# Performance work log

Hardware: AMD Instinct MI355X
Metric: run time of the kernel (lower is better)

The kernel has to match this reference:

```python
import jax, jax.numpy as jnp
import numpy as np

B, T = 4096, 16384
KLEN = 50          # min(50, n_steps) with dt=1
REFRACTORY = 3.0   # self.refractory / self.dt


def setup_inputs() -> dict:
    key = jax.random.key(0)
    k1, = jax.random.split(key, 1)
    # scale so that v_reset + I_filtered/100 can cross v_th (=-55 vs reset -70)
    I_input = jax.random.normal(k1, (B, T), dtype=jnp.float32) * 2000.0
    return {
        "I_input": I_input,
        "tau_m": jnp.float32(10.0),
        "tau_s": jnp.float32(5.0),
        "v_th": jnp.float32(-55.0),
        "v_reset": jnp.float32(-70.0),
        "eta": jnp.float32(-5.0),
    }


def _srm_spikes(I_input, tau_m, tau_s, v_th, v_reset, eta):
    # synaptic kernel: (exp(-t/tau_m) - exp(-t/tau_s)) / sum
    t = jnp.arange(KLEN, dtype=jnp.float32)
    kernel = jnp.exp(-t / tau_m) - jnp.exp(-t / tau_s)
    kernel = kernel / (jnp.sum(kernel) + 1e-10)
    # 'same' convolution per trace (np.convolve semantics: kernel flipped)
    I_filt = jax.vmap(lambda x: jnp.convolve(x, kernel, mode="same"))(I_input)

    def step(ref, I_t):
        # ref: [B] refractory countdown; I_t: [B] filtered current at time t
        in_ref = ref > 0
        v_free = v_reset + I_t / 100.0
        spike = jnp.where(jnp.logical_and(~in_ref, v_free >= v_th), 1.0, 0.0)
        new_ref = jnp.where(in_ref, ref - 1.0,
                            jnp.where(spike > 0, REFRACTORY, 0.0))
        return new_ref, spike

    ref0 = jnp.zeros((I_input.shape[0],), dtype=jnp.float32)
    # original loop runs t = 1 .. n_steps-1; spikes[0] stays 0
    _, spikes_t = jax.lax.scan(step, ref0, jnp.swapaxes(I_filt[:, 1:], 0, 1))
    spikes = jnp.concatenate(
        [jnp.zeros((I_input.shape[0], 1), dtype=jnp.float32),
         jnp.swapaxes(spikes_t, 0, 1)], axis=1)
    return spikes


def reference(I_input, tau_m, tau_s, v_th, v_reset, eta):
    return _srm_spikes(I_input, tau_m, tau_s, v_th, v_reset, eta)
```

## Files before the change

kernel.cpp:

```cpp
#include <hip/hip_runtime.h>


#define TLEN  16384
#define NROWS 4096
#define GRP   256
#define NGRP  64
#define KLEN  50
#define WPB   4
#define TILEW 336
#define CHK   2
#define GPC   (NGRP / CHK)

#define WS_FLAGS_OFF 256
#define WS_NEED (WS_FLAGS_OFF + (size_t)NROWS * CHK * sizeof(int))

typedef float f4 __attribute__((ext_vector_type(4)));

__device__ __forceinline__ float uniformf(float x) {
    return __int_as_float(__builtin_amdgcn_readfirstlane(__float_as_int(x)));
}

__device__ __forceinline__ int map_compose(int first, int then) {
    int r = 0;
#pragma unroll
    for (int s = 0; s < 4; ++s) {
        int a = (first >> (2 * s)) & 3;
        int b = (then >> (2 * a)) & 3;
        r |= b << (2 * s);
    }
    return r;
}

__device__ float solve_thresh(float v_reset, float v_th) {
    auto tokey = [](float f) {
        unsigned u = __float_as_uint(f);
        return (u & 0x80000000u) ? ~u : (u | 0x80000000u);
    };
    auto fromkey = [](unsigned k) {
        unsigned u = (k & 0x80000000u) ? (k & 0x7FFFFFFFu) : ~k;
        return __uint_as_float(u);
    };
    const float maxf = 3.402823466e38f;
    unsigned lo = tokey(-maxf), hi = tokey(maxf);
    if (!((v_reset + maxf / 100.0f) >= v_th))
        return __uint_as_float(0x7F800000u);
    while (lo < hi) {
        unsigned mid = lo + ((hi - lo) >> 1);
        float a = fromkey(mid);
        if ((v_reset + a / 100.0f) >= v_th) hi = mid;
        else lo = mid + 1;
    }
    return fromkey(lo);
}

__global__ __launch_bounds__(64)
void setup_kernel(const float* __restrict__ p_tau_m,
                  const float* __restrict__ p_tau_s,
                  const float* __restrict__ p_v_th,
                  const float* __restrict__ p_v_reset,
                  float* __restrict__ wsf)
{
    const int lane = threadIdx.x & 63;
    const float tau_m   = p_tau_m[0];
    const float tau_s   = p_tau_s[0];

    float ft = (float)lane;
    float v = (lane < KLEN) ? (expf(-ft / tau_m) - expf(-ft / tau_s)) : 0.0f;

    float ksum = 0.0f;
    for (int t = 0; t < KLEN; ++t)
        ksum += __shfl(v, t, 64);
    const float kden = ksum + 1e-10f;
    const float kt = v / kden;

    if (lane < KLEN) wsf[lane] = kt;
    if (lane == 0)   wsf[KLEN] = solve_thresh(p_v_reset[0], p_v_th[0]);
}

__global__ __launch_bounds__(256)
void conv_kernel(const float* __restrict__ I,
                 const float* __restrict__ wsf,
                 float* __restrict__ out,
                 int* __restrict__ flags)
{
    __shared__ __align__(16) float tile[WPB][2][TILEW];

    const int lane  = threadIdx.x & 63;
    const int wid   = threadIdx.x >> 6;
    const int w     = blockIdx.x * WPB + wid;
    const int row   = w >> 1;
    const int chunk = w & 1;
    const int gi0   = chunk * GPC;

    float kt[KLEN];
#pragma unroll
    for (int t = 0; t < KLEN; ++t) kt[t] = wsf[t];
    const float athr = wsf[KLEN];

    const float* Irow = I + (size_t)row * TLEN;
    float* Orow = out + (size_t)row * TLEN;

    float Cv[4], Nv[4], Lv[4];
    {
        f4 a = *(const f4*)(Irow + (size_t)gi0 * GRP + 4 * lane);
        Cv[0] = a.x; Cv[1] = a.y; Cv[2] = a.z; Cv[3] = a.w;
        f4 c = *(const f4*)(Irow + (size_t)(gi0 + 1) * GRP + 4 * lane);
        Nv[0] = c.x; Nv[1] = c.y; Nv[2] = c.z; Nv[3] = c.w;
    }

    if (lane < 8) {
        f4 h;
        if (chunk == 0) h = (f4){0.0f, 0.0f, 0.0f, 0.0f};
        else            h = *(const f4*)(Irow + (size_t)gi0 * GRP - 32 + 4 * lane);
        *(f4*)&tile[wid][0][4 * lane] = h;
    }
    {
        f4 c; c.x = Cv[0]; c.y = Cv[1]; c.z = Cv[2]; c.w = Cv[3];
        *(f4*)&tile[wid][0][32 + 4 * lane] = c;
    }

    int rowflag = 0;

    for (int g = 0; g < GPC; ++g) {
        const int cur = g & 1;
        const int nxt = cur ^ 1;
        const int gi  = gi0 + g;

        if (gi + 2 < NGRP) {
            f4 a = *(const f4*)(Irow + (size_t)(gi + 2) * GRP + 4 * lane);
            Lv[0] = a.x; Lv[1] = a.y; Lv[2] = a.z; Lv[3] = a.w;
        } else {
            Lv[0] = Lv[1] = Lv[2] = Lv[3] = 0.0f;
        }

        f4 nv; nv.x = Nv[0]; nv.y = Nv[1]; nv.z = Nv[2]; nv.w = Nv[3];
        if (lane < 8)
            *(f4*)&tile[wid][cur][288 + 4 * lane] = nv;
        *(f4*)&tile[wid][nxt][32 + 4 * lane] = nv;
        if (lane >= 56) {
            f4 cv; cv.x = Cv[0]; cv.y = Cv[1]; cv.z = Cv[2]; cv.w = Cv[3];
            *(f4*)&tile[wid][nxt][4 * (lane - 56)] = cv;
        }

        f4 wv[15];
#pragma unroll
        for (int i = 0; i < 15; ++i)
            wv[i] = *(const f4*)&tile[wid][cur][4 * lane + 4 + 4 * i];
#define WIN(m) (wv[(m) >> 2][(m) & 3])

        float acc[4];
        acc[0] = acc[1] = acc[2] = acc[3] = 0.0f;
#pragma unroll
        for (int o = -25; o <= 27; ++o) {
            const float w2 = WIN(o + 28);
#pragma unroll
            for (int k = 0; k < 4; ++k) {
                const int jj = k + 24 - o;
                if (jj >= 0 && jj < KLEN)
                    acc[k] = fmaf(kt[jj], w2, acc[k]);
            }
        }
#undef WIN

        const int tb = gi * GRP + 4 * lane;
        int cand[4];
#pragma unroll
        for (int k = 0; k < 4; ++k)
            cand[k] = (acc[k] >= athr) ? 1 : 0;
        cand[0] &= (tb != 0);

        rowflag |= cand[0] | cand[1] | cand[2] | cand[3];

        f4 o0;
        o0.x = cand[0] ? 1.0f : 0.0f;
        o0.y = cand[1] ? 1.0f : 0.0f;
        o0.z = cand[2] ? 1.0f : 0.0f;
        o0.w = cand[3] ? 1.0f : 0.0f;
        __builtin_nontemporal_store(o0, (f4*)(Orow + tb));

#pragma unroll
        for (int j = 0; j < 4; ++j) { Cv[j] = Nv[j]; Nv[j] = Lv[j]; }
    }

    const unsigned long long anyb = __ballot(rowflag != 0);
    if (lane == 0) flags[w] = (anyb != 0ULL) ? 1 : 0;
}

__global__ __launch_bounds__(256)
void fixup_kernel(const int* __restrict__ flags,
                  float* __restrict__ out)
{
    const int lane = threadIdx.x & 63;
    const int wid  = threadIdx.x >> 6;
    const int row  = blockIdx.x * WPB + wid;

    if ((flags[2 * row] | flags[2 * row + 1]) == 0) return;

    float* Orow = out + (size_t)row * TLEN;
    int r0 = 0;

    for (int g = 0; g < NGRP; ++g) {
        f4 o = *(const f4*)(Orow + g * GRP + 4 * lane);
        int cand[4];
        cand[0] = (o.x != 0.0f);
        cand[1] = (o.y != 0.0f);
        cand[2] = (o.z != 0.0f);
        cand[3] = (o.w != 0.0f);

        const int cm = cand[0] | cand[1] | cand[2] | cand[3];
        const unsigned long long anyc = __ballot(cm != 0);
        if (anyc == 0ULL) { r0 = 0; continue; }

        int s0 = 0, s1 = 1, s2 = 2, s3 = 3;
#pragma unroll
        for (int k = 0; k < 4; ++k) {
            const int c3 = cand[k] ? 3 : 0;
            s0 = (s0 > 0) ? (s0 - 1) : c3;
            s1 = (s1 > 0) ? (s1 - 1) : c3;
            s2 = (s2 > 0) ? (s2 - 1) : c3;
            s3 = (s3 > 0) ? (s3 - 1) : c3;
        }
        int P = s0 | (s1 << 2) | (s2 << 4) | (s3 << 6);

#pragma unroll
        for (int d = 1; d < 64; d <<= 1) {
            const int prev = __shfl_up(P, d, 64);
            const int comp = map_compose(prev, P);
            P = (lane >= d) ? comp : P;
        }
        const int Pprev = __shfl_up(P, 1, 64);
        const int sin0  = (lane == 0) ? r0 : ((Pprev >> (2 * r0)) & 3);
        const int Pfull = __shfl(P, 63, 64);
        r0 = (Pfull >> (2 * r0)) & 3;

        int s = sin0;
        float sp[4];
#pragma unroll
        for (int k = 0; k < 4; ++k) {
            const int spike = (s == 0) & cand[k];
            sp[k] = spike ? 1.0f : 0.0f;
            s = (s > 0) ? (s - 1) : (cand[k] ? 3 : 0);
        }
        f4 o0; o0.x = sp[0]; o0.y = sp[1]; o0.z = sp[2]; o0.w = sp[3];
        *(f4*)(Orow + g * GRP + 4 * lane) = o0;
    }
}

__global__ __launch_bounds__(256)
void srm_kernel(const float* __restrict__ I,
                const float* __restrict__ p_tau_m,
                const float* __restrict__ p_tau_s,
                const float* __restrict__ p_v_th,
                const float* __restrict__ p_v_reset,
                float* __restrict__ out)
{
    __shared__ __align__(16) float tile[WPB][2][TILEW];

    const int lane = threadIdx.x & 63;
    const int wid  = threadIdx.x >> 6;
    const int row  = blockIdx.x * WPB + wid;

    const float tau_m   = p_tau_m[0];
    const float tau_s   = p_tau_s[0];
    const float v_th    = p_v_th[0];
    const float v_reset = p_v_reset[0];

    float ku[KLEN];
    float ksum = 0.0f;
#pragma unroll
    for (int t = 0; t < KLEN; ++t) {
        float ft = (float)t;
        float v = expf(-ft / tau_m) - expf(-ft / tau_s);
        ksum += v;
        ku[t] = uniformf(v);
    }
    const float kden = uniformf(ksum + 1e-10f);
    float kt[KLEN];
#pragma unroll
    for (int t = 0; t < KLEN; ++t) kt[t] = uniformf(ku[t] / kden);

    const float athr = uniformf(solve_thresh(v_reset, v_th));

    const float* Irow = I + (size_t)row * TLEN;
    float* Orow = out + (size_t)row * TLEN;

    float Cv[4], Nv[4], Lv[4];
    {
        f4 a = *(const f4*)(Irow + 0 * GRP + 4 * lane);
        Cv[0] = a.x; Cv[1] = a.y; Cv[2] = a.z; Cv[3] = a.w;
        f4 c = *(const f4*)(Irow + 1 * GRP + 4 * lane);
        Nv[0] = c.x; Nv[1] = c.y; Nv[2] = c.z; Nv[3] = c.w;
    }

    if (lane < 8) {
        f4 z = (f4){0.0f, 0.0f, 0.0f, 0.0f};
        *(f4*)&tile[wid][0][4 * lane] = z;
    }
    {
        f4 c; c.x = Cv[0]; c.y = Cv[1]; c.z = Cv[2]; c.w = Cv[3];
        *(f4*)&tile[wid][0][32 + 4 * lane] = c;
    }

    int r0 = 0;

    for (int g = 0; g < NGRP; ++g) {
        const int cur = g & 1;
        const int nxt = cur ^ 1;

        if (g + 2 < NGRP) {
            f4 a = *(const f4*)(Irow + (size_t)(g + 2) * GRP + 4 * lane);
            Lv[0] = a.x; Lv[1] = a.y; Lv[2] = a.z; Lv[3] = a.w;
        } else {
            Lv[0] = Lv[1] = Lv[2] = Lv[3] = 0.0f;
        }

        f4 nv; nv.x = Nv[0]; nv.y = Nv[1]; nv.z = Nv[2]; nv.w = Nv[3];
        if (lane < 8)
            *(f4*)&tile[wid][cur][288 + 4 * lane] = nv;
        *(f4*)&tile[wid][nxt][32 + 4 * lane] = nv;
        if (lane >= 56) {
            f4 cv; cv.x = Cv[0]; cv.y = Cv[1]; cv.z = Cv[2]; cv.w = Cv[3];
            *(f4*)&tile[wid][nxt][4 * (lane - 56)] = cv;
        }

        f4 wv[15];
#pragma unroll
        for (int i = 0; i < 15; ++i)
            wv[i] = *(const f4*)&tile[wid][cur][4 * lane + 4 + 4 * i];
#define WIN(m) (wv[(m) >> 2][(m) & 3])

        float acc[4];
        acc[0] = acc[1] = acc[2] = acc[3] = 0.0f;
#pragma unroll
        for (int o = -25; o <= 27; ++o) {
            const float w = WIN(o + 28);
#pragma unroll
            for (int k = 0; k < 4; ++k) {
                const int jj = k + 24 - o;
                if (jj >= 0 && jj < KLEN)
                    acc[k] = fmaf(kt[jj], w, acc[k]);
            }
        }
#undef WIN

        const int tb = g * GRP + 4 * lane;
        int cand[4];
#pragma unroll
        for (int k = 0; k < 4; ++k)
            cand[k] = (acc[k] >= athr) ? 1 : 0;
        cand[0] &= (tb != 0);

        const int cm = cand[0] | cand[1] | cand[2] | cand[3];
        const unsigned long long anyc = __ballot(cm != 0);

        f4 o0;
        if (anyc == 0ULL) {
            o0 = (f4){0.0f, 0.0f, 0.0f, 0.0f};
            r0 = 0;
        } else {
            int s0 = 0, s1 = 1, s2 = 2, s3 = 3;
#pragma unroll
            for (int k = 0; k < 4; ++k) {
                const int c3 = cand[k] ? 3 : 0;
                s0 = (s0 > 0) ? (s0 - 1) : c3;
                s1 = (s1 > 0) ? (s1 - 1) : c3;
                s2 = (s2 > 0) ? (s2 - 1) : c3;
                s3 = (s3 > 0) ? (s3 - 1) : c3;
            }
            int P = s0 | (s1 << 2) | (s2 << 4) | (s3 << 6);
#pragma unroll
            for (int d = 1; d < 64; d <<= 1) {
                const int prev = __shfl_up(P, d, 64);
                const int comp = map_compose(prev, P);
                P = (lane >= d) ? comp : P;
            }
            const int Pprev = __shfl_up(P, 1, 64);
            const int sin0  = (lane == 0) ? r0 : ((Pprev >> (2 * r0)) & 3);
            const int Pfull = __shfl(P, 63, 64);
            r0 = (Pfull >> (2 * r0)) & 3;

            int s = sin0;
            float sp[4];
#pragma unroll
            for (int k = 0; k < 4; ++k) {
                const int spike = (s == 0) & cand[k];
                sp[k] = spike ? 1.0f : 0.0f;
                s = (s > 0) ? (s - 1) : (cand[k] ? 3 : 0);
            }
            o0.x = sp[0]; o0.y = sp[1]; o0.z = sp[2]; o0.w = sp[3];
        }

        __builtin_nontemporal_store(o0, (f4*)(Orow + tb));

#pragma unroll
        for (int j = 0; j < 4; ++j) { Cv[j] = Nv[j]; Nv[j] = Lv[j]; }
    }
}

extern "C" void kernel_launch(void* const* d_in, const int* in_sizes, int n_in,
                              void* d_out, int out_size, void* d_ws, size_t ws_size,
                              hipStream_t stream) {
    const float* I       = (const float*)d_in[0];
    const float* tau_m   = (const float*)d_in[1];
    const float* tau_s   = (const float*)d_in[2];
    const float* v_th    = (const float*)d_in[3];
    const float* v_reset = (const float*)d_in[4];
    float* out = (float*)d_out;

    if (ws_size >= WS_NEED) {
        float* wsf  = (float*)d_ws;
        int* flags  = (int*)((char*)d_ws + WS_FLAGS_OFF);
        setup_kernel<<<dim3(1), dim3(64), 0, stream>>>(
            tau_m, tau_s, v_th, v_reset, wsf);
        conv_kernel<<<dim3(NROWS * CHK / WPB), dim3(256), 0, stream>>>(
            I, wsf, out, flags);
        fixup_kernel<<<dim3(NROWS / WPB), dim3(256), 0, stream>>>(flags, out);
    } else {
        srm_kernel<<<dim3(NROWS / WPB), dim3(256), 0, stream>>>(
            I, tau_m, tau_s, v_th, v_reset, out);
    }
}
```

Before: 181.9 us.

## Widen conv tiles to 16 outputs per lane with swizzled LDS layout

The convolution kernel now has each lane compute 16 consecutive outputs over 1024-element groups instead of 4 outputs over 256-element groups. This amortizes shared-memory window reads across more FMAs, since each lane reads 17 vec4s for 16 outputs instead of 15 for 4. An XOR swizzle on LDS offsets is meant to avoid bank conflicts from the strided per-lane reads. Results are redistributed with shuffles so stores stay coalesced. In exchange, register pressure rises (16 accumulators plus 17 vec4 window registers), which may reduce occupancy, and the register-based prefetch pipeline is dropped.

```diff
diff --git a/kernel.cpp b/kernel.cpp
--- a/kernel.cpp
+++ b/kernel.cpp
@@ -3,13 +3,18 @@
 
 #define TLEN  16384
 #define NROWS 4096
-#define GRP   256
-#define NGRP  64
 #define KLEN  50
 #define WPB   4
+
+#define GRP   1024
+#define NGRP  16
+#define CHK   2
+#define GPC   8
+#define TILEB 272
+
+#define FGRP  256
+#define FNGRP 64
 #define TILEW 336
-#define CHK   2
-#define GPC   (NGRP / CHK)
 
 #define WS_FLAGS_OFF 256
 #define WS_NEED (WS_FLAGS_OFF + (size_t)NROWS * CHK * sizeof(int))
@@ -19,6 +24,8 @@
 __device__ __forceinline__ float uniformf(float x) {
     return __int_as_float(__builtin_amdgcn_readfirstlane(__float_as_int(x)));
 }
+
+__device__ __forceinline__ int swz(int blk) { return blk ^ ((blk >> 3) & 7); }
 
 __device__ __forceinline__ int map_compose(int first, int then) {
     int r = 0;
@@ -61,8 +68,8 @@
                   float* __restrict__ wsf)
 {
     const int lane = threadIdx.x & 63;
-    const float tau_m   = p_tau_m[0];
-    const float tau_s   = p_tau_s[0];
+    const float tau_m = p_tau_m[0];
+    const float tau_s = p_tau_s[0];
 
     float ft = (float)lane;
     float v = (lane < KLEN) ? (expf(-ft / tau_m) - expf(-ft / tau_s)) : 0.0f;
@@ -83,14 +90,13 @@
                  float* __restrict__ out,
                  int* __restrict__ flags)
 {
-    __shared__ __align__(16) float tile[WPB][2][TILEW];
+    __shared__ __align__(16) float tile[WPB][TILEB * 4];
 
     const int lane  = threadIdx.x & 63;
     const int wid   = threadIdx.x >> 6;
     const int w     = blockIdx.x * WPB + wid;
     const int row   = w >> 1;
     const int chunk = w & 1;
-    const int gi0   = chunk * GPC;
 
     float kt[KLEN];
 #pragma unroll
@@ -100,86 +106,81 @@
     const float* Irow = I + (size_t)row * TLEN;
     float* Orow = out + (size_t)row * TLEN;
 
-    float Cv[4], Nv[4], Lv[4];
-    {
-        f4 a = *(const f4*)(Irow + (size_t)gi0 * GRP + 4 * lane);
-        Cv[0] = a.x; Cv[1] = a.y; Cv[2] = a.z; Cv[3] = a.w;
-        f4 c = *(const f4*)(Irow + (size_t)(gi0 + 1) * GRP + 4 * lane);
-        Nv[0] = c.x; Nv[1] = c.y; Nv[2] = c.z; Nv[3] = c.w;
-    }
-
-    if (lane < 8) {
-        f4 h;
-        if (chunk == 0) h = (f4){0.0f, 0.0f, 0.0f, 0.0f};
-        else            h = *(const f4*)(Irow + (size_t)gi0 * GRP - 32 + 4 * lane);
-        *(f4*)&tile[wid][0][4 * lane] = h;
-    }
-    {
-        f4 c; c.x = Cv[0]; c.y = Cv[1]; c.z = Cv[2]; c.w = Cv[3];
-        *(f4*)&tile[wid][0][32 + 4 * lane] = c;
-    }
+    char* tb_ = (char*)&tile[wid][0];
+
+    int rdoff[17];
+#pragma unroll
+    for (int i = 0; i < 17; ++i) rdoff[i] = 16 * swz(4 * lane + i);
+    int wroff[4];
+#pragma unroll
+    for (int j = 0; j < 4; ++j) wroff[j] = 16 * swz(7 + lane + 64 * j);
+    const int hloff = 16 * swz(lane & 7);
+    const int hroff = 16 * swz(263 + ((lane - 56) & 7));
 
     int rowflag = 0;
 
     for (int g = 0; g < GPC; ++g) {
-        const int cur = g & 1;
-        const int nxt = cur ^ 1;
-        const int gi  = gi0 + g;
-
-        if (gi + 2 < NGRP) {
-            f4 a = *(const f4*)(Irow + (size_t)(gi + 2) * GRP + 4 * lane);
-            Lv[0] = a.x; Lv[1] = a.y; Lv[2] = a.z; Lv[3] = a.w;
-        } else {
-            Lv[0] = Lv[1] = Lv[2] = Lv[3] = 0.0f;
-        }
-
-        f4 nv; nv.x = Nv[0]; nv.y = Nv[1]; nv.z = Nv[2]; nv.w = Nv[3];
-        if (lane < 8)
-            *(f4*)&tile[wid][cur][288 + 4 * lane] = nv;
-        *(f4*)&tile[wid][nxt][32 + 4 * lane] = nv;
-        if (lane >= 56) {
-            f4 cv; cv.x = Cv[0]; cv.y = Cv[1]; cv.z = Cv[2]; cv.w = Cv[3];
-            *(f4*)&tile[wid][nxt][4 * (lane - 56)] = cv;
-        }
-
-        f4 wv[15];
-#pragma unroll
-        for (int i = 0; i < 15; ++i)
-            wv[i] = *(const f4*)&tile[wid][cur][4 * lane + 4 + 4 * i];
+        const int gi   = chunk * GPC + g;
+        const int base = gi * GRP;
+
+        f4 mv0 = *(const f4*)(Irow + base + 4 * lane);
+        f4 mv1 = *(const f4*)(Irow + base + 4 * lane + 256);
+        f4 mv2 = *(const f4*)(Irow + base + 4 * lane + 512);
+        f4 mv3 = *(const f4*)(Irow + base + 4 * lane + 768);
+        *(f4*)(tb_ + wroff[0]) = mv0;
+        *(f4*)(tb_ + wroff[1]) = mv1;
+        *(f4*)(tb_ + wroff[2]) = mv2;
+        *(f4*)(tb_ + wroff[3]) = mv3;
+        if (lane < 7) {
+            f4 h = (f4){0.0f, 0.0f, 0.0f, 0.0f};
+            if (gi > 0) h = *(const f4*)(Irow + base - 28 + 4 * lane);
+            *(f4*)(tb_ + hloff) = h;
+        }
+        if (lane >= 56 && lane < 62) {
+            f4 h = (f4){0.0f, 0.0f, 0.0f, 0.0f};
+            if (gi < NGRP - 1) h = *(const f4*)(Irow + base + GRP + 4 * (lane - 56));
+            *(f4*)(tb_ + hroff) = h;
+        }
+
+        f4 wv[17];
+#pragma unroll
+        for (int i = 0; i < 17; ++i)
+            wv[i] = *(const f4*)(tb_ + rdoff[i]);
 #define WIN(m) (wv[(m) >> 2][(m) & 3])
 
-        float acc[4];
-        acc[0] = acc[1] = acc[2] = acc[3] = 0.0f;
-#pragma unroll
-        for (int o = -25; o <= 27; ++o) {
-            const float w2 = WIN(o + 28);
-#pragma unroll
-            for (int k = 0; k < 4; ++k) {
+        float acc[16];
+#pragma unroll
+        for (int k = 0; k < 16; ++k) acc[k] = 0.0f;
+#pragma unroll
+        for (int o = -25; o <= 39; ++o) {
+            const float wx = WIN(o + 28);
+#pragma unroll
+            for (int k = 0; k < 16; ++k) {
                 const int jj = k + 24 - o;
                 if (jj >= 0 && jj < KLEN)
-                    acc[k] = fmaf(kt[jj], w2, acc[k]);
+                    acc[k] = fmaf(kt[jj], wx, acc[k]);
             }
         }
 #undef WIN
 
-        const int tb = gi * GRP + 4 * lane;
-        int cand[4];
-#pragma unroll
-        for (int k = 0; k < 4; ++k)
-            cand[k] = (acc[k] >= athr) ? 1 : 0;
-        cand[0] &= (tb != 0);
-
-        rowflag |= cand[0] | cand[1] | cand[2] | cand[3];
-
-        f4 o0;
-        o0.x = cand[0] ? 1.0f : 0.0f;
-        o0.y = cand[1] ? 1.0f : 0.0f;
-        o0.z = cand[2] ? 1.0f : 0.0f;
-        o0.w = cand[3] ? 1.0f : 0.0f;
-        __builtin_nontemporal_store(o0, (f4*)(Orow + tb));
-
-#pragma unroll
-        for (int j = 0; j < 4; ++j) { Cv[j] = Nv[j]; Nv[j] = Lv[j]; }
+        int m16 = 0;
+#pragma unroll
+        for (int k = 0; k < 16; ++k)
+            m16 |= (acc[k] >= athr) ? (1 << k) : 0;
+        if (base + 16 * lane == 0) m16 &= ~1;
+        rowflag |= m16;
+
+        const int sh = 4 * (lane & 3);
+#pragma unroll
+        for (int j = 0; j < 4; ++j) {
+            const int bits = __shfl(m16, (lane >> 2) + 16 * j, 64);
+            f4 o0;
+            o0.x = ((bits >> (sh + 0)) & 1) ? 1.0f : 0.0f;
+            o0.y = ((bits >> (sh + 1)) & 1) ? 1.0f : 0.0f;
+            o0.z = ((bits >> (sh + 2)) & 1) ? 1.0f : 0.0f;
+            o0.w = ((bits >> (sh + 3)) & 1) ? 1.0f : 0.0f;
+            __builtin_nontemporal_store(o0, (f4*)(Orow + base + 4 * lane + 256 * j));
+        }
     }
 
     const unsigned long long anyb = __ballot(rowflag != 0);
@@ -199,8 +200,8 @@
     float* Orow = out + (size_t)row * TLEN;
     int r0 = 0;
 
-    for (int g = 0; g < NGRP; ++g) {
-        f4 o = *(const f4*)(Orow + g * GRP + 4 * lane);
+    for (int g = 0; g < FNGRP; ++g) {
+        f4 o = *(const f4*)(Orow + g * FGRP + 4 * lane);
         int cand[4];
         cand[0] = (o.x != 0.0f);
         cand[1] = (o.y != 0.0f);
@@ -242,7 +243,7 @@
             s = (s > 0) ? (s - 1) : (cand[k] ? 3 : 0);
         }
         f4 o0; o0.x = sp[0]; o0.y = sp[1]; o0.z = sp[2]; o0.w = sp[3];
-        *(f4*)(Orow + g * GRP + 4 * lane) = o0;
+        *(f4*)(Orow + g * FGRP + 4 * lane) = o0;
     }
 }
 
@@ -286,9 +287,9 @@
 
     float Cv[4], Nv[4], Lv[4];
     {
-        f4 a = *(const f4*)(Irow + 0 * GRP + 4 * lane);
+        f4 a = *(const f4*)(Irow + 0 * FGRP + 4 * lane);
         Cv[0] = a.x; Cv[1] = a.y; Cv[2] = a.z; Cv[3] = a.w;
-        f4 c = *(const f4*)(Irow + 1 * GRP + 4 * lane);
+        f4 c = *(const f4*)(Irow + 1 * FGRP + 4 * lane);
         Nv[0] = c.x; Nv[1] = c.y; Nv[2] = c.z; Nv[3] = c.w;
     }
 
@@ -303,12 +304,12 @@
 
     int r0 = 0;
 
-    for (int g = 0; g < NGRP; ++g) {
+    for (int g = 0; g < FNGRP; ++g) {
         const int cur = g & 1;
         const int nxt = cur ^ 1;
 
-        if (g + 2 < NGRP) {
-            f4 a = *(const f4*)(Irow + (size_t)(g + 2) * GRP + 4 * lane);
+        if (g + 2 < FNGRP) {
+            f4 a = *(const f4*)(Irow + (size_t)(g + 2) * FGRP + 4 * lane);
             Lv[0] = a.x; Lv[1] = a.y; Lv[2] = a.z; Lv[3] = a.w;
         } else {
             Lv[0] = Lv[1] = Lv[2] = Lv[3] = 0.0f;
@@ -343,7 +344,7 @@
         }
 #undef WIN
 
-        const int tb = g * GRP + 4 * lane;
+        const int tb = g * FGRP + 4 * lane;
         int cand[4];
 #pragma unroll
         for (int k = 0; k < 4; ++k)
```

Result: slower. 220.4 us (+21.1%).
